# Performance work log

Measured on AMD Instinct MI355X. Metric: run time of the kernel, lower is better.

## Reference

```python
import jax, jax.numpy as jnp
import numpy as np

N_NODES = 20000
N_EDGES = 640000
IN_DIM = 128
HEADS = 4
C1 = 64      # hidden_dim1
C2 = 128     # hidden_dim2 (gat2, 1 head)
GRU = 128
PW = 15      # pred_window


def gat_layer(x, src, dst, W, a_src, a_dst, bias):
    # PyG GATConv (eval mode, self-loops already appended): linear -> per-edge
    # LeakyReLU(0.2) attention -> segment softmax over dst -> scatter-sum.
    n = x.shape[0]
    heads, ch = a_src.shape
    xl = (x @ W).reshape(n, heads, ch)                      # [N,H,C]
    al = jnp.sum(xl * a_src, axis=-1)                       # [N,H]
    ar = jnp.sum(xl * a_dst, axis=-1)                       # [N,H]
    e = jax.nn.leaky_relu(al[src] + ar[dst], 0.2)           # [E,H]
    m = jax.ops.segment_max(e, dst, num_segments=n)
    ee = jnp.exp(e - m[dst])
    s = jax.ops.segment_sum(ee, dst, num_segments=n)
    alpha = ee / s[dst]                                     # [E,H]
    msg = xl[src] * alpha[:, :, None]                       # [E,H,C]
    out = jax.ops.segment_sum(msg, dst, num_segments=n)
    return out.reshape(n, heads * ch) + bias


def gru_cell(x, h, W_ih, W_hh, b_ih, b_hh):
    gi = x @ W_ih.T + b_ih
    gh = h @ W_hh.T + b_hh
    ir, iz, ih = jnp.split(gi, 3, axis=1)
    hr, hz, hn = jnp.split(gh, 3, axis=1)
    r = jax.nn.sigmoid(ir + hr)
    z = jax.nn.sigmoid(iz + hz)
    n = jnp.tanh(ih + r * hn)
    return (1.0 - z) * n + z * h


def setup_inputs() -> dict:
    key = jax.random.key(0)
    ks = jax.random.split(key, 24)
    f = jnp.float32
    sc = 0.05
    inp = {
        'dynamic': jax.random.normal(ks[0], (N_NODES, IN_DIM), dtype=f),
        'edge_index': jax.random.randint(ks[1], (2, N_EDGES), 0, N_NODES, dtype=jnp.int32),
        'cI': jax.random.uniform(ks[2], (N_NODES,), dtype=f),
        'cR': jax.random.uniform(ks[3], (N_NODES,), dtype=f),
        'Npop': jnp.ones((N_NODES, 1), dtype=f) * 1e6,
        'I': jax.random.uniform(ks[4], (N_NODES,), dtype=f) * 100.0,
        'R': jax.random.uniform(ks[5], (N_NODES,), dtype=f) * 100.0,
        'dI': jax.random.normal(ks[6], (N_NODES,), dtype=f),
        'dR': jax.random.normal(ks[7], (N_NODES,), dtype=f),
        # gat1
        'W1': jax.random.normal(ks[8], (IN_DIM, HEADS * C1), dtype=f) * sc,
        'a_src1': jax.random.normal(ks[9], (HEADS, C1), dtype=f) * sc,
        'a_dst1': jax.random.normal(ks[10], (HEADS, C1), dtype=f) * sc,
        'b1': jnp.zeros((HEADS * C1,), dtype=f),
        # gat2 (1 head)
        'W2': jax.random.normal(ks[11], (HEADS * C1, C2), dtype=f) * sc,
        'a_src2': jax.random.normal(ks[12], (1, C2), dtype=f) * sc,
        'a_dst2': jax.random.normal(ks[13], (1, C2), dtype=f) * sc,
        'b2': jnp.zeros((C2,), dtype=f),
        # GRUCell
        'W_ih': jax.random.normal(ks[14], (3 * GRU, C2), dtype=f) * sc,
        'W_hh': jax.random.normal(ks[15], (3 * GRU, GRU), dtype=f) * sc,
        'b_ih': jnp.zeros((3 * GRU,), dtype=f),
        'b_hh': jnp.zeros((3 * GRU,), dtype=f),
        # output heads
        'W_I': jax.random.normal(ks[16], (PW, GRU + 2), dtype=f) * sc,
        'b_I': jnp.zeros((PW,), dtype=f),
        'W_R': jax.random.normal(ks[17], (PW, GRU + 2), dtype=f) * sc,
        'b_R': jnp.zeros((PW,), dtype=f),
        'W_sir': jax.random.normal(ks[18], (2, GRU + 2), dtype=f) * sc,
        'b_sir': jnp.zeros((2,), dtype=f),
    }
    return inp


def reference(dynamic, edge_index, cI, cR, Npop, I, R, dI, dR,
              W1, a_src1, a_dst1, b1, W2, a_src2, a_dst2, b2,
              W_ih, W_hh, b_ih, b_hh, W_I, b_I, W_R, b_R, W_sir, b_sir):
    n = dynamic.shape[0]
    loops = jnp.arange(n, dtype=edge_index.dtype)
    src = jnp.concatenate([edge_index[0], loops])   # PyG add_self_loops=True
    dst = jnp.concatenate([edge_index[1], loops])

    x = jax.nn.elu(gat_layer(dynamic, src, dst, W1, a_src1, a_dst1, b1))
    x = jax.nn.elu(gat_layer(x, src, dst, W2, a_src2, a_dst2, b2))

    h = gru_cell(x, jnp.zeros((n, GRU), dtype=x.dtype), W_ih, W_hh, b_ih, b_hh)
    hc = jnp.concatenate([h, cI[:, None], cR[:, None]], axis=1)
    pred_I = hc @ W_I.T + b_I
    pred_R = hc @ W_R.T + b_R
    pred_res = hc @ W_sir.T + b_sir
    alpha = jax.nn.sigmoid(pred_res[:, 0])
    beta = jax.nn.sigmoid(pred_res[:, 1])

    Nv = Npop[:, 0]
    S = Nv - I - R
    phy_I, phy_R = [], []
    for _ in range(PW):
        dI_val = alpha * I * (S / Nv) - beta * I
        dR_val = beta * I
        phy_I.append(dI_val)
        phy_R.append(dR_val)
        I = I + jax.lax.stop_gradient(dI_val)
        R = R + jax.lax.stop_gradient(dR_val)
    phy_I = jnp.stack(phy_I, axis=1)
    phy_R = jnp.stack(phy_R, axis=1)
    return pred_I, pred_R, phy_I, phy_R, h
```

## Files before the change

kernel.cpp:

```cpp
#include <hip/hip_runtime.h>

#define NN 20000
#define NE 640000
#define NET (NE + NN)
#define NB 256
#define RR 79
#define NSL 256
#define ESL4 625

typedef __attribute__((ext_vector_type(8))) short bf16x8;
typedef __attribute__((ext_vector_type(4))) float f32x4;
typedef __attribute__((ext_vector_type(2))) float f32x2;

__device__ inline ushort f2bf_rne(float x) {
    unsigned u = __float_as_uint(x);
    return (ushort)((u + 0x7FFFu + ((u >> 16) & 1u)) >> 16);
}
__device__ inline float bf2f(ushort u) {
    return __uint_as_float(((unsigned)u) << 16);
}
__device__ inline void split2(float x, ushort& hi, ushort& lo) {
    unsigned u = __float_as_uint(x);
    unsigned r = (u + 0x7FFFu + ((u >> 16) & 1u)) & 0xFFFF0000u;
    hi = (ushort)(r >> 16);
    lo = f2bf_rne(x - __uint_as_float(r));
}
__device__ inline float rlane(float x, int k) {
    return __int_as_float(__builtin_amdgcn_readlane(__float_as_int(x), k));
}


__global__ void csrA_kernel(const int* __restrict__ ei, ushort* __restrict__ cnt,
                            const float* __restrict__ W1, const float* __restrict__ as1,
                            const float* __restrict__ ad1, float* __restrict__ w1f,
                            const float* __restrict__ W2, const float* __restrict__ as2,
                            const float* __restrict__ ad2, float* __restrict__ w2f,
                            const float* __restrict__ W_ih,
                            const float* __restrict__ W_I, const float* __restrict__ b_I,
                            const float* __restrict__ W_R, const float* __restrict__ b_R,
                            const float* __restrict__ W_sir, const float* __restrict__ b_sir,
                            ushort* __restrict__ w1fh, ushort* __restrict__ w1fl,
                            ushort* __restrict__ w2fh, ushort* __restrict__ w2fl,
                            ushort* __restrict__ w3fh, ushort* __restrict__ w3fl,
                            ushort* __restrict__ wtfh, ushort* __restrict__ wtfl,
                            float* __restrict__ wc, float* __restrict__ wb) {
    int b = blockIdx.x, t = threadIdx.x;
    if (b < NSL) {
        __shared__ int h[NB];
        h[t] = 0;
        __syncthreads();
        const int4* d4 = (const int4*)(ei + NE);
        for (int i = t; i < ESL4; i += 256) {
            int4 d = d4[b * ESL4 + i];
            atomicAdd(&h[(unsigned)d.x / RR], 1);
            atomicAdd(&h[(unsigned)d.y / RR], 1);
            atomicAdd(&h[(unsigned)d.z / RR], 1);
            atomicAdd(&h[(unsigned)d.w / RR], 1);
        }
        __syncthreads();
        cnt[t * NSL + b] = (ushort)h[t];
    } else if (b == NSL) {
        if (t < 128) {
            int k = t;
#pragma unroll
            for (int hh = 0; hh < 4; hh++) {
                float s1 = 0.f, s2 = 0.f;
                for (int c = 0; c < 64; c++) {
                    float w = W1[k * 256 + hh * 64 + c];
                    s1 += w * as1[hh * 64 + c];
                    s2 += w * ad1[hh * 64 + c];
                }
                w1f[k * 8 + hh] = s1;
                w1f[k * 8 + 4 + hh] = s2;
            }
        }
    } else if (b == NSL + 1) {
        int k = t;
        float s1 = 0.f, s2 = 0.f;
        for (int c = 0; c < 128; c++) {
            float w = W2[k * 128 + c];
            s1 += w * as2[c];
            s2 += w * ad2[c];
        }
        w2f[k * 2] = s1;
        w2f[k * 2 + 1] = s2;
    } else if (b == NSL + 2) {
        if (t < 32) {
            int p = t;
            const float* Wr = (p < 15) ? W_I + p * 130
                            : (p < 30) ? W_R + (p - 15) * 130
                                       : W_sir + (p - 30) * 130;
            wc[p * 2] = Wr[128];
            wc[p * 2 + 1] = Wr[129];
            wb[p] = (p < 15) ? b_I[p] : (p < 30) ? b_R[p - 15] : b_sir[p - 30];
        }
    } else {
        int pb = b - (NSL + 3);
        if (pb < 16) {
            int base = pb * 2048;
#pragma unroll
            for (int q = 0; q < 8; q++) {
                int i = base + t + q * 256;
                int j = i & 7, ln = (i >> 3) & 63, rem = i >> 9;
                int k32 = rem & 3, n16 = rem >> 2;
                int k = k32 * 32 + ((ln >> 4) << 3) + j;
                int n = n16 * 16 + (ln & 15);
                ushort h, l; split2(W1[k * 256 + n], h, l);
                w1fh[i] = h; w1fl[i] = l;
            }
        } else if (pb < 32) {
            int base = (pb - 16) * 2048;
#pragma unroll
            for (int q = 0; q < 8; q++) {
                int i = base + t + q * 256;
                int j = i & 7, ln = (i >> 3) & 63, rem = i >> 9;
                int k32 = rem & 7, n16 = rem >> 3;
                int k = k32 * 32 + ((ln >> 4) << 3) + j;
                int n = n16 * 16 + (ln & 15);
                ushort h, l; split2(W2[k * 128 + n], h, l);
                w2fh[i] = h; w2fl[i] = l;
            }
        } else if (pb < 56) {
            int base = (pb - 32) * 2048;
#pragma unroll
            for (int q = 0; q < 8; q++) {
                int i = base + t + q * 256;
                int j = i & 7, ln = (i >> 3) & 63, rem = i >> 9;
                int k32 = rem & 3, n16 = rem >> 2;
                int k = k32 * 32 + ((ln >> 4) << 3) + j;
                int n = n16 * 16 + (ln & 15);
                ushort h, l; split2(W_ih[n * 128 + k], h, l);
                w3fh[i] = h; w3fl[i] = l;
            }
        } else {
            int base = (pb - 56) * 2048;
#pragma unroll
            for (int q = 0; q < 8; q++) {
                int i = base + t + q * 256;
                int j = i & 7, ln = (i >> 3) & 63, rem = i >> 9;
                int k32 = rem & 3, n16 = rem >> 2;
                int k = k32 * 32 + ((ln >> 4) << 3) + j;
                int n = n16 * 16 + (ln & 15);
                const float* Wr = (n < 15) ? W_I + n * 130
                                : (n < 30) ? W_R + (n - 15) * 130
                                           : W_sir + (n - 30) * 130;
                ushort h, l; split2(Wr[k], h, l);
                wtfh[i] = h; wtfl[i] = l;
            }
        }
    }
}

__global__ void csrB_kernel(const ushort* __restrict__ cnt, int* __restrict__ sbase) {
    __shared__ int ws1[16], ws2[16];
    int t = threadIdx.x, wv = t >> 6, ln = t & 63;
    int base = t * 64;
    int loc[64];
    int run = 0;
    const ushort4* c4 = (const ushort4*)(cnt + base);
#pragma unroll
    for (int q = 0; q < 16; q++) {
        ushort4 v = c4[q];
        loc[q * 4 + 0] = run; run += v.x;
        loc[q * 4 + 1] = run; run += v.y;
        loc[q * 4 + 2] = run; run += v.z;
        loc[q * 4 + 3] = run; run += v.w;
    }
    int s = run;
#pragma unroll
    for (int o = 1; o < 64; o <<= 1) { int u = __shfl_up(s, o, 64); if (ln >= o) s += u; }
    if (ln == 63) ws1[wv] = s;
    __syncthreads();
    if (t < 16) {
        int sv = ws1[t];
#pragma unroll
        for (int o = 1; o < 16; o <<= 1) { int u = __shfl_up(sv, o, 16); if (t >= o) sv += u; }
        ws2[t] = sv;
    }
    __syncthreads();
    int excl = (wv ? ws2[wv - 1] : 0) + s - run;
#pragma unroll
    for (int q = 0; q < 64; q++) sbase[base + q] = excl + loc[q];
}

__global__ void csrC_kernel(const int* __restrict__ ei, const int* __restrict__ sbase,
                            int* __restrict__ ebuf, const float* __restrict__ X,
                            const float* __restrict__ wf, ushort* __restrict__ Xbf,
                            float* __restrict__ al, float* __restrict__ ar) {
    int b = blockIdx.x, t = threadIdx.x;
    if (b < NSL) {
        __shared__ int cur[NB];
        cur[t] = sbase[t * NSL + b];
        __syncthreads();
        const int4* s4 = (const int4*)ei;
        const int4* d4 = (const int4*)(ei + NE);
        for (int i = t; i < ESL4; i += 256) {
            int4 sv = s4[b * ESL4 + i];
            int4 dv = d4[b * ESL4 + i];
            int p;
            p = atomicAdd(&cur[(unsigned)dv.x / RR], 1); ebuf[p] = sv.x | (dv.x << 15);
            p = atomicAdd(&cur[(unsigned)dv.y / RR], 1); ebuf[p] = sv.y | (dv.y << 15);
            p = atomicAdd(&cur[(unsigned)dv.z / RR], 1); ebuf[p] = sv.z | (dv.z << 15);
            p = atomicAdd(&cur[(unsigned)dv.w / RR], 1); ebuf[p] = sv.w | (dv.w << 15);
        }
    } else {
        __shared__ float ws[8][128];
        for (int i = t; i < 1024; i += 256) ws[i & 7][i >> 3] = wf[i];
        __syncthreads();
        int wv = t >> 6, ln = t & 63;
        int n = (b - NSL) * 4 + wv;
        float2 xv = *(const float2*)(X + (size_t)n * 128 + ln * 2);
        ushort2 ub;
        ub.x = f2bf_rne(xv.x);
        ub.y = f2bf_rne(xv.y);
        *(ushort2*)(Xbf + (size_t)n * 128 + ln * 2) = ub;
        float p[8];
#pragma unroll
        for (int o = 0; o < 8; o++) p[o] = xv.x * ws[o][ln * 2] + xv.y * ws[o][ln * 2 + 1];
#pragma unroll
        for (int off = 32; off > 0; off >>= 1)
#pragma unroll
            for (int o = 0; o < 8; o++) p[o] += __shfl_xor(p[o], off, 64);
        if (ln == 0) {
#pragma unroll
            for (int h = 0; h < 4; h++) {
                al[n * 4 + h] = p[h];
                ar[n * 4 + h] = p[4 + h];
            }
        }
    }
}

__global__ void csrD_kernel(const int* __restrict__ ebuf, const int* __restrict__ sbase,
                            int* __restrict__ offs, int* __restrict__ csr_src) {
    __shared__ int hist[RR], lcur[RR];
    int b = blockIdx.x, t = threadIdx.x;
    int lo = b * RR;
    int Ra = min(RR, NN - lo);
    if (Ra <= 0) { if (b == 0 && t == 255) offs[NN] = NET; return; }
    int e0 = sbase[b * NSL];
    int e1 = (b < NB - 1) ? sbase[(b + 1) * NSL] : NE;
    int m = e1 - e0;
    for (int i = t; i < Ra; i += 256) hist[i] = 0;
    __syncthreads();
    for (int j = t; j < m; j += 256) atomicAdd(&hist[(ebuf[e0 + j] >> 15) - lo], 1);
    __syncthreads();
    if (t < 64) {
        int cbase = e0 + lo;
        int carry = 0;
#pragma unroll
        for (int c = 0; c < 2; c++) {
            int i = c * 64 + t;
            int v = (i < Ra) ? hist[i] + 1 : 0;
            int s = v;
#pragma unroll
            for (int o = 1; o < 64; o <<= 1) { int u = __shfl_up(s, o, 64); if (t >= o) s += u; }
            if (i < Ra) {
                int off = cbase + carry + s - v;
                offs[lo + i] = off;
                lcur[i] = off;
            }
            carry += __shfl(s, 63, 64);
        }
    }
    if (b == 0 && t == 255) offs[NN] = NET;
    __syncthreads();
    for (int i = t; i < Ra; i += 256) csr_src[lcur[i] + hist[i]] = lo + i;
    __syncthreads();
    for (int j = t; j < m; j += 256) {
        int p = ebuf[e0 + j];
        int pos = atomicAdd(&lcur[(p >> 15) - lo], 1);
        csr_src[pos] = p & 0x7FFF;
    }
}

template <int H, bool FUSE>
__launch_bounds__(256)
__global__ void gat_gather_w(const ushort* __restrict__ X, const float* __restrict__ al,
                             const float* __restrict__ ar, const int* __restrict__ offs,
                             const int* __restrict__ csr, const float* __restrict__ bias,
                             void* __restrict__ outp) {
    int t = threadIdx.x;
    int wv = t >> 6, ln = t & 63;
    int n = blockIdx.x * 4 + wv;
    int e0 = offs[n], e1 = offs[n + 1];

    float arv[H], srun[H];
    f32x2 acc2[H];
#pragma unroll
    for (int h = 0; h < H; h++) {
        arv[h] = ar[n * H + h];
        srun[h] = 0.f;
        acc2[h][0] = 0.f; acc2[h][1] = 0.f;
    }
    const ushort* Xc = X + ln * 2;

    for (int base = e0; base < e1; base += 64) {
        int cnt = e1 - base; if (cnt > 64) cnt = 64;
        bool vld = ln < cnt;
        int src = vld ? csr[base + ln] : 0;
        float wgt[H];
        {
            float av[H];
            if (H == 4) {
                float4 a4 = *(const float4*)(al + (size_t)src * 4);
                av[0] = a4.x; av[H > 1 ? 1 : 0] = a4.y;
                av[H > 2 ? 2 : 0] = a4.z; av[H > 3 ? 3 : 0] = a4.w;
            } else {
                av[0] = al[src];
            }
#pragma unroll
            for (int h = 0; h < H; h++) {
                float lg = av[h] + arv[h];
                lg = lg > 0.f ? lg : 0.2f * lg;
                wgt[h] = vld ? __expf(lg) : 0.f;
            }
        }
        float ls[H];
#pragma unroll
        for (int h = 0; h < H; h++) ls[h] = wgt[h];
#pragma unroll
        for (int off = 32; off > 0; off >>= 1)
#pragma unroll
            for (int h = 0; h < H; h++) ls[h] += __shfl_xor(ls[h], off, 64);
#pragma unroll
        for (int h = 0; h < H; h++) srun[h] += ls[h];

        int k = 0;
        for (; k + 16 <= cnt; k += 16) {
            int s[16];
            unsigned u[16];
#pragma unroll
            for (int q = 0; q < 16; q++) s[q] = __builtin_amdgcn_readlane(src, k + q);
#pragma unroll
            for (int q = 0; q < 16; q++) u[q] = *(const unsigned*)(Xc + (size_t)s[q] * 128);
#pragma unroll
            for (int q = 0; q < 16; q++) {
                f32x2 xv;
                xv[0] = __uint_as_float(u[q] << 16);
                xv[1] = __uint_as_float(u[q] & 0xffff0000u);
#pragma unroll
                for (int h = 0; h < H; h++) {
                    float w = rlane(wgt[h], k + q);
                    f32x2 ww; ww[0] = w; ww[1] = w;
                    acc2[h] = __builtin_elementwise_fma(ww, xv, acc2[h]);
                }
            }
        }
        for (; k + 8 <= cnt; k += 8) {
            int s[8];
            unsigned u[8];
#pragma unroll
            for (int q = 0; q < 8; q++) s[q] = __builtin_amdgcn_readlane(src, k + q);
#pragma unroll
            for (int q = 0; q < 8; q++) u[q] = *(const unsigned*)(Xc + (size_t)s[q] * 128);
#pragma unroll
            for (int q = 0; q < 8; q++) {
                f32x2 xv;
                xv[0] = __uint_as_float(u[q] << 16);
                xv[1] = __uint_as_float(u[q] & 0xffff0000u);
#pragma unroll
                for (int h = 0; h < H; h++) {
                    float w = rlane(wgt[h], k + q);
                    f32x2 ww; ww[0] = w; ww[1] = w;
                    acc2[h] = __builtin_elementwise_fma(ww, xv, acc2[h]);
                }
            }
        }
        for (; k < cnt; k++) {
            int s0 = __builtin_amdgcn_readlane(src, k);
            unsigned u0 = *(const unsigned*)(Xc + (size_t)s0 * 128);
            f32x2 xv;
            xv[0] = __uint_as_float(u0 << 16);
            xv[1] = __uint_as_float(u0 & 0xffff0000u);
#pragma unroll
            for (int h = 0; h < H; h++) {
                float w = rlane(wgt[h], k);
                f32x2 ww; ww[0] = w; ww[1] = w;
                acc2[h] = __builtin_elementwise_fma(ww, xv, acc2[h]);
            }
        }
    }
    if (FUSE) {
        ushort* out = (ushort*)outp;
        float inv = 1.f / srun[0];
        float v0 = acc2[0][0] * inv + bias[ln * 2];
        float v1 = acc2[0][1] * inv + bias[ln * 2 + 1];
        v0 = v0 > 0.f ? v0 : __expf(v0) - 1.f;
        v1 = v1 > 0.f ? v1 : __expf(v1) - 1.f;
        ushort2 o;
        o.x = f2bf_rne(v0);
        o.y = f2bf_rne(v1);
        *(ushort2*)(out + (size_t)n * 128 + ln * 2) = o;
    } else {
        ushort* out = (ushort*)outp;
#pragma unroll
        for (int h = 0; h < H; h++) {
            float inv = 1.f / srun[h];
            ushort2 o;
            o.x = f2bf_rne(acc2[h][0] * inv);
            o.y = f2bf_rne(acc2[h][1] * inv);
            *(ushort2*)(out + (size_t)n * (H * 128) + h * 128 + ln * 2) = o;
        }
    }
}

template <int ACT, bool OUTBF, bool ALAR, int NF>
__launch_bounds__(256)
__global__ void gemm_fr(const ushort* __restrict__ A, const ushort* __restrict__ Bfh,
                        const ushort* __restrict__ Bfl, const float* __restrict__ bias,
                        void* __restrict__ Cptr, int M, int K, int lda, int ldc,
                        int zA, int zB, int zC, const float* __restrict__ w2f,
                        float* __restrict__ al2, float* __restrict__ ar2) {
    __shared__ ushort Ah[64 * 64];
    __shared__ float s_w2f[ALAR ? 256 : 1][2];
    int tid = threadIdx.x;
    int z = blockIdx.z;
    int bm = blockIdx.x * 64;
    int ny = blockIdx.y * (64 * NF);
    int wid = tid >> 6, ln = tid & 63;
    int K32v = K >> 5;
    const bf16x8* BfhV = (const bf16x8*)Bfh;
    const bf16x8* BflV = (const bf16x8*)Bfl;
    f32x4 acc[4][NF];
#pragma unroll
    for (int a = 0; a < 4; a++)
#pragma unroll
        for (int nf = 0; nf < NF; nf++)
#pragma unroll
            for (int j = 0; j < 4; j++) acc[a][nf][j] = 0.f;
    float p0a[4], p1a[4];
    bool do_alar = ALAR && blockIdx.y == 0;
    if (ALAR) {
#pragma unroll
        for (int i = 0; i < 4; i++) { p0a[i] = 0.f; p1a[i] = 0.f; }
        s_w2f[tid][0] = w2f[tid * 2];
        s_w2f[tid][1] = w2f[tid * 2 + 1];
        __syncthreads();
    }
    size_t abase = (size_t)z * zA;
    int ct[NF];
#pragma unroll
    for (int nf = 0; nf < NF; nf++)
        ct[nf] = (z * zB + ny + wid * (16 * NF) + nf * 16) >> 4;

    for (int k0 = 0; k0 < K; k0 += 64) {
#pragma unroll
        for (int i = 0; i < 4; i++) {
            int idx = tid + i * 256;
            int r = idx >> 4, c4 = (idx & 15) * 4;
            int gr = bm + r;
            ushort4 v = make_ushort4(0, 0, 0, 0);
            if (gr < M) v = *(const ushort4*)(A + abase + (size_t)gr * lda + k0 + c4);
            int ab = (r * 128 + c4 * 2) ^ ((r & 7) << 4);
            *(ushort4*)((char*)Ah + ab) = v;
            if (ALAR && do_alar) {
                int kk = k0 + c4;
                float x0 = bf2f(v.x), x1 = bf2f(v.y), x2 = bf2f(v.z), x3 = bf2f(v.w);
                p0a[i] = fmaf(x0, s_w2f[kk][0], p0a[i]);
                p0a[i] = fmaf(x1, s_w2f[kk + 1][0], p0a[i]);
                p0a[i] = fmaf(x2, s_w2f[kk + 2][0], p0a[i]);
                p0a[i] = fmaf(x3, s_w2f[kk + 3][0], p0a[i]);
                p1a[i] = fmaf(x0, s_w2f[kk][1], p1a[i]);
                p1a[i] = fmaf(x1, s_w2f[kk + 1][1], p1a[i]);
                p1a[i] = fmaf(x2, s_w2f[kk + 2][1], p1a[i]);
                p1a[i] = fmaf(x3, s_w2f[kk + 3][1], p1a[i]);
            }
        }
        __syncthreads();
#pragma unroll
        for (int ks = 0; ks < 2; ks++) {
            int k32 = (k0 >> 5) + ks;
            int kb = ks * 64 + (ln >> 4) * 16;
#pragma unroll
            for (int nf = 0; nf < NF; nf++) {
                size_t fb = (size_t)(ct[nf] * K32v + k32) * 64 + ln;
                bf16x8 bh = BfhV[fb];
                bf16x8 bl = BflV[fb];
#pragma unroll
                for (int mf = 0; mf < 4; mf++) {
                    int r = mf * 16 + (ln & 15);
                    int ab = (r * 128 + kb) ^ ((r & 7) << 4);
                    bf16x8 ah = *(bf16x8*)((char*)Ah + ab);
                    acc[mf][nf] = __builtin_amdgcn_mfma_f32_16x16x32_bf16(ah, bh, acc[mf][nf], 0, 0, 0);
                    acc[mf][nf] = __builtin_amdgcn_mfma_f32_16x16x32_bf16(ah, bl, acc[mf][nf], 0, 0, 0);
                }
            }
        }
        __syncthreads();
    }
    if (ALAR && do_alar) {
#pragma unroll
        for (int i = 0; i < 4; i++) {
            float p0 = p0a[i], p1 = p1a[i];
#pragma unroll
            for (int off = 8; off > 0; off >>= 1) {
                p0 += __shfl_xor(p0, off, 16);
                p1 += __shfl_xor(p1, off, 16);
            }
            if ((tid & 15) == 0) {
                int gr = bm + (tid >> 4) + i * 16;
                if (gr < M) { al2[gr] = p0; ar2[gr] = p1; }
            }
        }
    }
    float* Cf = (float*)Cptr;
    ushort* Cu = (ushort*)Cptr;
#pragma unroll
    for (int nf = 0; nf < NF; nf++) {
        int colL = ny + wid * (16 * NF) + nf * 16 + (ln & 15);
#pragma unroll
        for (int mf = 0; mf < 4; mf++) {
#pragma unroll
            for (int j = 0; j < 4; j++) {
                int row = bm + mf * 16 + (ln >> 4) * 4 + j;
                if (row < M) {
                    float v = acc[mf][nf][j];
                    if (ACT) {
                        v += bias[z * zC + colL];
                        v = v > 0.f ? v : (__expf(v) - 1.f);
                    }
                    size_t ci = (size_t)row * ldc + z * zC + colL;
                    if (OUTBF) Cu[ci] = f2bf_rne(v);
                    else       Cf[ci] = v;
                }
            }
        }
    }
}

__launch_bounds__(256)
__global__ void tail_kernel(const ushort* __restrict__ gi, const float* __restrict__ b_ih,
                            const float* __restrict__ b_hh, const ushort* __restrict__ wtfh,
                            const ushort* __restrict__ wtfl, const float* __restrict__ wc,
                            const float* __restrict__ wb, const float* __restrict__ cI,
                            const float* __restrict__ cR, const float* __restrict__ Npop,
                            const float* __restrict__ I0, const float* __restrict__ R0,
                            float* __restrict__ out_h, float* __restrict__ predI,
                            float* __restrict__ predR, float* __restrict__ phyI,
                            float* __restrict__ phyR) {
    __shared__ ushort As[64 * 128];
    __shared__ float s_ab[2][64];
    __shared__ float s_ci[64], s_cr[64];
    int t = threadIdx.x;
    int bm = blockIdx.x * 64;
    int wid = t >> 6, ln = t & 63;
    const bf16x8* WTh = (const bf16x8*)wtfh;
    const bf16x8* WTl = (const bf16x8*)wtfl;
    if (t < 64) {
        int n = bm + t;
        s_ci[t] = (n < NN) ? cI[n] : 0.f;
        s_cr[t] = (n < NN) ? cR[n] : 0.f;
    }
    for (int i = t; i < 2048; i += 256) {
        int r = i >> 5, c4 = (i & 31) * 4;
        int n = bm + r;
        ushort4 ua = make_ushort4(0, 0, 0, 0), ub = ua, uc = ua;
        if (n < NN) {
            const ushort* g = gi + (size_t)n * 384;
            ua = *(const ushort4*)(g + c4);
            ub = *(const ushort4*)(g + 128 + c4);
            uc = *(const ushort4*)(g + 256 + c4);
        }
        float gaa[4] = {bf2f(ua.x), bf2f(ua.y), bf2f(ua.z), bf2f(ua.w)};
        float gba[4] = {bf2f(ub.x), bf2f(ub.y), bf2f(ub.z), bf2f(ub.w)};
        float gca[4] = {bf2f(uc.x), bf2f(uc.y), bf2f(uc.z), bf2f(uc.w)};
        float hv[4];
#pragma unroll
        for (int q = 0; q < 4; q++) {
            int c = c4 + q;
            float rr = 1.f / (1.f + __expf(-(gaa[q] + b_ih[c] + b_hh[c])));
            float zz = 1.f / (1.f + __expf(-(gba[q] + b_ih[128 + c] + b_hh[128 + c])));
            float xx = gca[q] + b_ih[256 + c] + rr * b_hh[256 + c];
            xx = fminf(fmaxf(xx, -15.f), 15.f);
            float e2 = __expf(2.f * xx);
            hv[q] = (1.f - zz) * (e2 - 1.f) / (e2 + 1.f);
        }
        if (n < NN)
            *(float4*)(out_h + (size_t)n * 128 + c4) = make_float4(hv[0], hv[1], hv[2], hv[3]);
        ushort4 hb = make_ushort4(f2bf_rne(hv[0]), f2bf_rne(hv[1]), f2bf_rne(hv[2]), f2bf_rne(hv[3]));
        int ab = (r * 256 + c4 * 2) ^ ((r & 7) << 4);
        *(ushort4*)((char*)As + ab) = hb;
    }
    __syncthreads();
    f32x4 acc2[2];
#pragma unroll
    for (int nf = 0; nf < 2; nf++)
#pragma unroll
        for (int j = 0; j < 4; j++) acc2[nf][j] = 0.f;
#pragma unroll
    for (int ks = 0; ks < 4; ks++) {
        int r = wid * 16 + (ln & 15);
        int abyte = (r * 256 + ks * 64 + (ln >> 4) * 16) ^ ((r & 7) << 4);
        bf16x8 ah = *(bf16x8*)((char*)As + abyte);
#pragma unroll
        for (int nf = 0; nf < 2; nf++) {
            size_t fb = (size_t)(nf * 4 + ks) * 64 + ln;
            bf16x8 bh = WTh[fb];
            bf16x8 bl = WTl[fb];
            acc2[nf] = __builtin_amdgcn_mfma_f32_16x16x32_bf16(ah, bh, acc2[nf], 0, 0, 0);
            acc2[nf] = __builtin_amdgcn_mfma_f32_16x16x32_bf16(ah, bl, acc2[nf], 0, 0, 0);
        }
    }
#pragma unroll
    for (int nf = 0; nf < 2; nf++) {
        int col = nf * 16 + (ln & 15);
#pragma unroll
        for (int j = 0; j < 4; j++) {
            int rl = wid * 16 + (ln >> 4) * 4 + j;
            int n = bm + rl;
            float v = acc2[nf][j] + s_ci[rl] * wc[col * 2] + s_cr[rl] * wc[col * 2 + 1] + wb[col];
            if (n < NN) {
                if (col < 15)      predI[(size_t)n * 15 + col] = v;
                else if (col < 30) predR[(size_t)n * 15 + col - 15] = v;
            }
            if (col == 30) s_ab[0][rl] = v;
            if (col == 31) s_ab[1][rl] = v;
        }
    }
    __syncthreads();
    if (t < 64) {
        int n = bm + t;
        if (n < NN) {
            float alpha = 1.f / (1.f + __expf(-s_ab[0][t]));
            float beta  = 1.f / (1.f + __expf(-s_ab[1][t]));
            float Nv = Npop[n];
            float Iv = I0[n], Rv = R0[n];
            float SoN = (Nv - Iv - Rv) / Nv;
            for (int st = 0; st < 15; st++) {
                float dI = alpha * Iv * SoN - beta * Iv;
                float dR = beta * Iv;
                phyI[(size_t)n * 15 + st] = dI;
                phyR[(size_t)n * 15 + st] = dR;
                Iv += dI; Rv += dR;
            }
        }
    }
}

extern "C" void kernel_launch(void* const* d_in, const int* in_sizes, int n_in,
                              void* d_out, int out_size, void* d_ws, size_t ws_size,
                              hipStream_t stream) {
    const float* dynamic = (const float*)d_in[0];
    const int*   ei      = (const int*)d_in[1];
    const float* cI      = (const float*)d_in[2];
    const float* cR      = (const float*)d_in[3];
    const float* Npop    = (const float*)d_in[4];
    const float* I0      = (const float*)d_in[5];
    const float* R0      = (const float*)d_in[6];
    const float* W1      = (const float*)d_in[9];
    const float* a_src1  = (const float*)d_in[10];
    const float* a_dst1  = (const float*)d_in[11];
    const float* b1      = (const float*)d_in[12];
    const float* W2      = (const float*)d_in[13];
    const float* a_src2  = (const float*)d_in[14];
    const float* a_dst2  = (const float*)d_in[15];
    const float* b2      = (const float*)d_in[16];
    const float* W_ih    = (const float*)d_in[17];
    const float* b_ih    = (const float*)d_in[19];
    const float* b_hh    = (const float*)d_in[20];
    const float* W_I     = (const float*)d_in[21];
    const float* b_I     = (const float*)d_in[22];
    const float* W_R     = (const float*)d_in[23];
    const float* b_R     = (const float*)d_in[24];
    const float* W_sir   = (const float*)d_in[25];
    const float* b_sir   = (const float*)d_in[26];
    float* out = (float*)d_out;
    float* out_predI = out;
    float* out_predR = out + 300000;
    float* out_phyI  = out + 600000;
    float* out_phyR  = out + 900000;
    float* out_h     = out + 1200000;

    int* wsi = (int*)d_ws;
    int* offs    = wsi;
    int* csr_src = wsi + 20096;
    ushort* cnt  = (ushort*)(wsi + 680192);
    int* sbase   = wsi + 712960;
    float* fp = (float*)(wsi + 778496);
    float* w1f = fp; fp += 1152;
    float* w2f = fp; fp += 512;
    float* wc  = fp; fp += 64;
    float* wb  = fp; fp += 64;
    float* al1 = fp; fp += 80128;
    float* ar1 = fp; fp += 80128;
    float* al2 = fp; fp += 20096;
    float* ar2 = fp; fp += 20096;
    ushort* wub  = (ushort*)fp; fp += 118784;
    ushort* w1fh = wub;
    ushort* w1fl = wub + 32768;
    ushort* w2fh = wub + 65536;
    ushort* w2fl = wub + 98304;
    ushort* w3fh = wub + 131072;
    ushort* w3fl = wub + 180224;
    ushort* wtfh = wub + 229376;
    ushort* wtfl = wub + 233472;
    ushort* dyn_bf = (ushort*)fp; fp += 1280000;
    ushort* x1u = (ushort*)fp; fp += 2560000;
    ushort* x2u = x1u;
    float* R  = fp; fp += 7680000;
    int* ebuf = (int*)R;
    ushort* agg_bf = (ushort*)R;
    ushort* xl2_bf = (ushort*)R;
    ushort* gi_bf  = (ushort*)R;

    csrA_kernel<<<NSL + 3 + 58, 256, 0, stream>>>(ei, cnt, W1, a_src1, a_dst1, w1f,
                                                  W2, a_src2, a_dst2, w2f, W_ih,
                                                  W_I, b_I, W_R, b_R, W_sir, b_sir,
                                                  w1fh, w1fl, w2fh, w2fl, w3fh, w3fl,
                                                  wtfh, wtfl, wc, wb);
    csrB_kernel<<<1, 1024, 0, stream>>>(cnt, sbase);
    csrC_kernel<<<NSL + 5000, 256, 0, stream>>>(ei, sbase, ebuf, dynamic, w1f,
                                                dyn_bf, al1, ar1);
    csrD_kernel<<<NB, 256, 0, stream>>>(ebuf, sbase, offs, csr_src);

    gat_gather_w<4, false><<<5000, 256, 0, stream>>>(dyn_bf, al1, ar1, offs, csr_src, nullptr, agg_bf);
    gemm_fr<1, true, false, 1><<<dim3(313, 1, 4), 256, 0, stream>>>(
        agg_bf, w1fh, w1fl, b1, x1u, NN, 128, 512, 256, 128, 64, 64,
        nullptr, nullptr, nullptr);

    gemm_fr<0, true, true, 1><<<dim3(313, 2, 1), 256, 0, stream>>>(
        x1u, w2fh, w2fl, nullptr, xl2_bf, NN, 256, 256, 128, 0, 0, 0,
        w2f, al2, ar2);
    gat_gather_w<1, true><<<5000, 256, 0, stream>>>(xl2_bf, al2, ar2, offs, csr_src, b2, x2u);

    gemm_fr<0, true, false, 2><<<dim3(313, 1, 3), 256, 0, stream>>>(
        x2u, w3fh, w3fl, nullptr, gi_bf, NN, 128, 128, 384, 0, 128, 128,
        nullptr, nullptr, nullptr);

    tail_kernel<<<313, 256, 0, stream>>>(gi_bf, b_ih, b_hh, wtfh, wtfl, wc, wb,
                                         cI, cR, Npop, I0, R0, out_h,
                                         out_predI, out_predR, out_phyI, out_phyR);
}
```

Measured before the change: 171.2 us.

## Fuse layer-1 projection GEMM and layer-2 linear/attention GEMM into one kernel

Replaces the two back-to-back GEMM launches (per-head layer-1 projection with bias+ELU, then the layer-2 linear with attention logits) with one kernel. It keeps the 64x256 ELU output tile in shared memory and feeds it straight into the second GEMM. This removes the global write and read of the intermediate x1 activation and one launch. In exchange, the grid shrinks to 313 blocks with about 48KB of shared memory each, which reduces parallelism and occupancy, and the layer-1 heads are now processed serially inside each block.

```diff
diff --git a/kernel.cpp b/kernel.cpp
--- a/kernel.cpp
+++ b/kernel.cpp
@@ -405,15 +405,146 @@
     }
 }
 
-template <int ACT, bool OUTBF, bool ALAR, int NF>
+__launch_bounds__(256)
+__global__ void gat_mlp_kernel(const ushort* __restrict__ agg,
+                               const ushort* __restrict__ w1fh, const ushort* __restrict__ w1fl,
+                               const float* __restrict__ b1,
+                               const ushort* __restrict__ w2fh, const ushort* __restrict__ w2fl,
+                               const float* __restrict__ w2f,
+                               ushort* __restrict__ xl2, float* __restrict__ al2,
+                               float* __restrict__ ar2) {
+    __shared__ ushort Ast[64 * 128];
+    __shared__ ushort X1[64 * 256];
+    __shared__ float s_w2f[256][2];
+    int t = threadIdx.x;
+    int bm = blockIdx.x * 64;
+    int wid = t >> 6, ln = t & 63;
+    const bf16x8* B1h = (const bf16x8*)w1fh;
+    const bf16x8* B1l = (const bf16x8*)w1fl;
+    const bf16x8* B2h = (const bf16x8*)w2fh;
+    const bf16x8* B2l = (const bf16x8*)w2fl;
+    s_w2f[t][0] = w2f[t * 2];
+    s_w2f[t][1] = w2f[t * 2 + 1];
+
+    for (int z = 0; z < 4; z++) {
+        __syncthreads();
+        for (int i = t; i < 2048; i += 256) {
+            int r = i >> 5, c4 = (i & 31) * 4;
+            int gr = bm + r;
+            ushort4 v = make_ushort4(0, 0, 0, 0);
+            if (gr < NN) v = *(const ushort4*)(agg + (size_t)gr * 512 + z * 128 + c4);
+            int ab = (r * 256 + c4 * 2) ^ ((r & 7) << 4);
+            *(ushort4*)((char*)Ast + ab) = v;
+        }
+        __syncthreads();
+        f32x4 acc[4];
+#pragma unroll
+        for (int mf = 0; mf < 4; mf++)
+#pragma unroll
+            for (int j = 0; j < 4; j++) acc[mf][j] = 0.f;
+        int ct1 = z * 4 + wid;
+#pragma unroll
+        for (int k32 = 0; k32 < 4; k32++) {
+            size_t fb = (size_t)(ct1 * 4 + k32) * 64 + ln;
+            bf16x8 bh = B1h[fb];
+            bf16x8 bl = B1l[fb];
+            int kb = k32 * 64 + (ln >> 4) * 16;
+#pragma unroll
+            for (int mf = 0; mf < 4; mf++) {
+                int r = mf * 16 + (ln & 15);
+                int ab = (r * 256 + kb) ^ ((r & 7) << 4);
+                bf16x8 ah = *(bf16x8*)((char*)Ast + ab);
+                acc[mf] = __builtin_amdgcn_mfma_f32_16x16x32_bf16(ah, bh, acc[mf], 0, 0, 0);
+                acc[mf] = __builtin_amdgcn_mfma_f32_16x16x32_bf16(ah, bl, acc[mf], 0, 0, 0);
+            }
+        }
+        int col = z * 64 + wid * 16 + (ln & 15);
+        float bb = b1[col];
+#pragma unroll
+        for (int mf = 0; mf < 4; mf++)
+#pragma unroll
+            for (int j = 0; j < 4; j++) {
+                int r = mf * 16 + (ln >> 4) * 4 + j;
+                float v = acc[mf][j] + bb;
+                v = v > 0.f ? v : (__expf(v) - 1.f);
+                int ab = (r * 512 + col * 2) ^ ((r & 7) << 4);
+                *(ushort*)((char*)X1 + ab) = f2bf_rne(v);
+            }
+    }
+    __syncthreads();
+
+    {
+        int r = t >> 2, q = t & 3;
+        float p0 = 0.f, p1 = 0.f;
+        for (int c4 = q * 64; c4 < q * 64 + 64; c4 += 4) {
+            int ab = (r * 512 + c4 * 2) ^ ((r & 7) << 4);
+            ushort4 v = *(ushort4*)((char*)X1 + ab);
+            float x0 = bf2f(v.x), x1v = bf2f(v.y), x2v = bf2f(v.z), x3v = bf2f(v.w);
+            p0 = fmaf(x0, s_w2f[c4][0], p0);
+            p0 = fmaf(x1v, s_w2f[c4 + 1][0], p0);
+            p0 = fmaf(x2v, s_w2f[c4 + 2][0], p0);
+            p0 = fmaf(x3v, s_w2f[c4 + 3][0], p0);
+            p1 = fmaf(x0, s_w2f[c4][1], p1);
+            p1 = fmaf(x1v, s_w2f[c4 + 1][1], p1);
+            p1 = fmaf(x2v, s_w2f[c4 + 2][1], p1);
+            p1 = fmaf(x3v, s_w2f[c4 + 3][1], p1);
+        }
+        p0 += __shfl_xor(p0, 1, 4);
+        p0 += __shfl_xor(p0, 2, 4);
+        p1 += __shfl_xor(p1, 1, 4);
+        p1 += __shfl_xor(p1, 2, 4);
+        if (q == 0) {
+            int n = bm + r;
+            if (n < NN) { al2[n] = p0; ar2[n] = p1; }
+        }
+    }
+
+    f32x4 acc2[4][2];
+#pragma unroll
+    for (int mf = 0; mf < 4; mf++)
+#pragma unroll
+        for (int nf = 0; nf < 2; nf++)
+#pragma unroll
+            for (int j = 0; j < 4; j++) acc2[mf][nf][j] = 0.f;
+#pragma unroll
+    for (int k32 = 0; k32 < 8; k32++) {
+        int kb = k32 * 64 + (ln >> 4) * 16;
+#pragma unroll
+        for (int nf = 0; nf < 2; nf++) {
+            int ct = wid * 2 + nf;
+            size_t fb = (size_t)(ct * 8 + k32) * 64 + ln;
+            bf16x8 bh = B2h[fb];
+            bf16x8 bl = B2l[fb];
+#pragma unroll
+            for (int mf = 0; mf < 4; mf++) {
+                int r = mf * 16 + (ln & 15);
+                int ab = (r * 512 + kb) ^ ((r & 7) << 4);
+                bf16x8 ah = *(bf16x8*)((char*)X1 + ab);
+                acc2[mf][nf] = __builtin_amdgcn_mfma_f32_16x16x32_bf16(ah, bh, acc2[mf][nf], 0, 0, 0);
+                acc2[mf][nf] = __builtin_amdgcn_mfma_f32_16x16x32_bf16(ah, bl, acc2[mf][nf], 0, 0, 0);
+            }
+        }
+    }
+#pragma unroll
+    for (int nf = 0; nf < 2; nf++) {
+        int col = wid * 32 + nf * 16 + (ln & 15);
+#pragma unroll
+        for (int mf = 0; mf < 4; mf++)
+#pragma unroll
+            for (int j = 0; j < 4; j++) {
+                int row = bm + mf * 16 + (ln >> 4) * 4 + j;
+                if (row < NN) xl2[(size_t)row * 128 + col] = f2bf_rne(acc2[mf][nf][j]);
+            }
+    }
+}
+
+template <int ACT, bool OUTBF, int NF>
 __launch_bounds__(256)
 __global__ void gemm_fr(const ushort* __restrict__ A, const ushort* __restrict__ Bfh,
                         const ushort* __restrict__ Bfl, const float* __restrict__ bias,
                         void* __restrict__ Cptr, int M, int K, int lda, int ldc,
-                        int zA, int zB, int zC, const float* __restrict__ w2f,
-                        float* __restrict__ al2, float* __restrict__ ar2) {
+                        int zA, int zB, int zC) {
     __shared__ ushort Ah[64 * 64];
-    __shared__ float s_w2f[ALAR ? 256 : 1][2];
     int tid = threadIdx.x;
     int z = blockIdx.z;
     int bm = blockIdx.x * 64;
@@ -429,15 +560,6 @@
         for (int nf = 0; nf < NF; nf++)
 #pragma unroll
             for (int j = 0; j < 4; j++) acc[a][nf][j] = 0.f;
-    float p0a[4], p1a[4];
-    bool do_alar = ALAR && blockIdx.y == 0;
-    if (ALAR) {
-#pragma unroll
-        for (int i = 0; i < 4; i++) { p0a[i] = 0.f; p1a[i] = 0.f; }
-        s_w2f[tid][0] = w2f[tid * 2];
-        s_w2f[tid][1] = w2f[tid * 2 + 1];
-        __syncthreads();
-    }
     size_t abase = (size_t)z * zA;
     int ct[NF];
 #pragma unroll
@@ -454,18 +576,6 @@
             if (gr < M) v = *(const ushort4*)(A + abase + (size_t)gr * lda + k0 + c4);
             int ab = (r * 128 + c4 * 2) ^ ((r & 7) << 4);
             *(ushort4*)((char*)Ah + ab) = v;
-            if (ALAR && do_alar) {
-                int kk = k0 + c4;
-                float x0 = bf2f(v.x), x1 = bf2f(v.y), x2 = bf2f(v.z), x3 = bf2f(v.w);
-                p0a[i] = fmaf(x0, s_w2f[kk][0], p0a[i]);
-                p0a[i] = fmaf(x1, s_w2f[kk + 1][0], p0a[i]);
-                p0a[i] = fmaf(x2, s_w2f[kk + 2][0], p0a[i]);
-                p0a[i] = fmaf(x3, s_w2f[kk + 3][0], p0a[i]);
-                p1a[i] = fmaf(x0, s_w2f[kk][1], p1a[i]);
-                p1a[i] = fmaf(x1, s_w2f[kk + 1][1], p1a[i]);
-                p1a[i] = fmaf(x2, s_w2f[kk + 2][1], p1a[i]);
-                p1a[i] = fmaf(x3, s_w2f[kk + 3][1], p1a[i]);
-            }
         }
         __syncthreads();
 #pragma unroll
@@ -488,21 +598,6 @@
             }
         }
         __syncthreads();
-    }
-    if (ALAR && do_alar) {
-#pragma unroll
-        for (int i = 0; i < 4; i++) {
-            float p0 = p0a[i], p1 = p1a[i];
-#pragma unroll
-            for (int off = 8; off > 0; off >>= 1) {
-                p0 += __shfl_xor(p0, off, 16);
-                p1 += __shfl_xor(p1, off, 16);
-            }
-            if ((tid & 15) == 0) {
-                int gr = bm + (tid >> 4) + i * 16;
-                if (gr < M) { al2[gr] = p0; ar2[gr] = p1; }
-            }
-        }
     }
     float* Cf = (float*)Cptr;
     ushort* Cu = (ushort*)Cptr;
@@ -696,8 +791,7 @@
     ushort* wtfh = wub + 229376;
     ushort* wtfl = wub + 233472;
     ushort* dyn_bf = (ushort*)fp; fp += 1280000;
-    ushort* x1u = (ushort*)fp; fp += 2560000;
-    ushort* x2u = x1u;
+    ushort* x2u = (ushort*)fp; fp += 1280000;
     float* R  = fp; fp += 7680000;
     int* ebuf = (int*)R;
     ushort* agg_bf = (ushort*)R;
@@ -715,18 +809,12 @@
     csrD_kernel<<<NB, 256, 0, stream>>>(ebuf, sbase, offs, csr_src);
 
     gat_gather_w<4, false><<<5000, 256, 0, stream>>>(dyn_bf, al1, ar1, offs, csr_src, nullptr, agg_bf);
-    gemm_fr<1, true, false, 1><<<dim3(313, 1, 4), 256, 0, stream>>>(
-        agg_bf, w1fh, w1fl, b1, x1u, NN, 128, 512, 256, 128, 64, 64,
-        nullptr, nullptr, nullptr);
-
-    gemm_fr<0, true, true, 1><<<dim3(313, 2, 1), 256, 0, stream>>>(
-        x1u, w2fh, w2fl, nullptr, xl2_bf, NN, 256, 256, 128, 0, 0, 0,
-        w2f, al2, ar2);
+    gat_mlp_kernel<<<313, 256, 0, stream>>>(agg_bf, w1fh, w1fl, b1, w2fh, w2fl, w2f,
+                                            xl2_bf, al2, ar2);
     gat_gather_w<1, true><<<5000, 256, 0, stream>>>(xl2_bf, al2, ar2, offs, csr_src, b2, x2u);
 
-    gemm_fr<0, true, false, 2><<<dim3(313, 1, 3), 256, 0, stream>>>(
-        x2u, w3fh, w3fl, nullptr, gi_bf, NN, 128, 128, 384, 0, 128, 128,
-        nullptr, nullptr, nullptr);
+    gemm_fr<0, true, 2><<<dim3(313, 1, 3), 256, 0, stream>>>(
+        x2u, w3fh, w3fl, nullptr, gi_bf, NN, 128, 128, 384, 0, 128, 128);
 
     tail_kernel<<<313, 256, 0, stream>>>(gi_bf, b_ih, b_hh, wtfh, wtfl, wc, wb,
                                          cI, cR, Npop, I0, R0, out_h,
```

After: 171.4 us. No clear change (+0.1%).
